# Kernel optimization log

Hardware: AMD Instinct MI355X
Metric: run time of the kernel (lower is better)

Reference implementation:

```python
import jax, jax.numpy as jnp
import numpy as np

N_NODES = 50000
N_EDGES = 400000
D = 128


def _rgg_layer(x, src, tgt, Wk, Wq, Wv, Ws, b, n_nodes):
    # Node-level projections (dense GEMMs, as in PyG which applies Linear before message passing)
    k = x @ Wk  # lin_key, gathered at targets
    q = x @ Wq  # lin_query, gathered at sources
    v = x @ Wv  # lin_value, gathered at sources
    # Per-edge gather + sigmoid gate + elementwise message
    eta = jax.nn.sigmoid(k[tgt] + q[src])  # [E, D]
    msg = eta * v[src]                      # [E, D]
    # Scatter-add aggregation to target nodes
    agg = jax.ops.segment_sum(msg, tgt, num_segments=n_nodes)
    # Root/skip connection + bias
    return agg + x @ Ws + b


def setup_inputs() -> dict:
    key = jax.random.key(0)
    ks = jax.random.split(key, 12)
    s = 1.0 / np.sqrt(D)
    x = jax.random.normal(ks[0], (N_NODES, D), dtype=jnp.float32)
    edge_index = jax.random.randint(ks[1], (2, N_EDGES), 0, N_NODES, dtype=jnp.int64)
    W = lambda k: (jax.random.normal(k, (D, D), dtype=jnp.float32) * s)
    return {
        "x": x,
        "edge_index": edge_index,
        "Wk1": W(ks[2]), "Wq1": W(ks[3]), "Wv1": W(ks[4]), "Ws1": W(ks[5]),
        "b1": jnp.zeros((D,), dtype=jnp.float32),
        "Wk2": W(ks[6]), "Wq2": W(ks[7]), "Wv2": W(ks[8]), "Ws2": W(ks[9]),
        "b2": jnp.zeros((D,), dtype=jnp.float32),
    }


def reference(x, edge_index, Wk1, Wq1, Wv1, Ws1, b1, Wk2, Wq2, Wv2, Ws2, b2):
    src, tgt = edge_index[0], edge_index[1]
    n = x.shape[0]
    h = _rgg_layer(x, src, tgt, Wk1, Wq1, Wv1, Ws1, b1, n)
    h = jax.nn.relu(h)
    # F.dropout treated as identity (deterministic/inference reference)
    out = _rgg_layer(h, src, tgt, Wk2, Wq2, Wv2, Ws2, b2, n)
    return out
```

## Files before the change

### kernel.cpp

```cpp
#include <hip/hip_runtime.h>

#define N_NODES 50000
#define D 128
#define N_EDGES 400000
#define NCHUNKS ((N_NODES + 255) / 256)
#define NBLK64 ((N_NODES + 63) / 64)
#define W_FRAG_SHORTS 16384

#define MW_BLOCKS  64
#define HIST_BLOCKS ((N_EDGES + 255) / 256)
#define PREP_BLOCKS (MW_BLOCKS + HIST_BLOCKS)

typedef short s8v  __attribute__((ext_vector_type(8)));
typedef float f4v  __attribute__((ext_vector_type(4)));

__device__ __forceinline__ unsigned int f2bf(float f) {
    unsigned int u = __float_as_uint(f);
    u += 0x7FFFu + ((u >> 16) & 1u);
    return u >> 16;
}
__device__ __forceinline__ unsigned int packbf(float a, float b) {
    return (f2bf(b) << 16) | f2bf(a);
}
__device__ __forceinline__ float bflo(unsigned int u) { return __uint_as_float(u << 16); }
__device__ __forceinline__ float bfhi(unsigned int u) { return __uint_as_float(u & 0xFFFF0000u); }
__device__ __forceinline__ float sigm(float x) {
    return __builtin_amdgcn_rcpf(1.f + __expf(-x));
}

__global__ __launch_bounds__(256)
void prep_all(const float* __restrict__ W0, const float* __restrict__ W1,
              const float* __restrict__ W2, const float* __restrict__ W3,
              const float* __restrict__ W4, const float* __restrict__ W5,
              const float* __restrict__ W6, const float* __restrict__ W7,
              short* __restrict__ Wt,
              const int* __restrict__ tgt, int* __restrict__ counts)
{
    const int b = blockIdx.x;
    if (b < MW_BLOCKS) {
        const int wsel = b >> 3;
        const float* W = (wsel == 0) ? W0 : (wsel == 1) ? W1 : (wsel == 2) ? W2 :
                         (wsel == 3) ? W3 : (wsel == 4) ? W4 : (wsel == 5) ? W5 :
                         (wsel == 6) ? W6 : W7;
        const int slot = (b & 7) * 256 + threadIdx.x;
        const int frag = slot >> 6;
        const int lane = slot & 63;
        const int n    = (frag >> 2) * 16 + (lane & 15);
        const int kc   = frag & 3;
        const int quad = lane >> 4;
        const int k0   = kc * 32 + quad * 8;
        s8v v;
#pragma unroll
        for (int j = 0; j < 8; ++j)
            v[j] = (short)f2bf(W[(size_t)(k0 + j) * D + n]);
        *(s8v*)(Wt + (size_t)wsel * W_FRAG_SHORTS + (size_t)slot * 8) = v;
    } else {
        const int e = (b - MW_BLOCKS) * 256 + threadIdx.x;
        if (e < N_EDGES) atomicAdd(&counts[tgt[e]], 1);
    }
}

__global__ __launch_bounds__(256)
void csr_scan(const int* __restrict__ counts, int* __restrict__ off,
              int* __restrict__ cursor, int* __restrict__ done_ctr,
              int* __restrict__ chunk_sum)
{
    __shared__ int s[256];
    const int b = blockIdx.x, t = threadIdx.x;
    const int i = b * 256 + t;
    const int v = (i < N_NODES) ? counts[i] : 0;
    s[t] = v;
    __syncthreads();
    for (int d = 1; d < 256; d <<= 1) {
        int tt = (t >= d) ? s[t - d] : 0;
        __syncthreads();
        s[t] += tt;
        __syncthreads();
    }
    const int incl = s[t];

    if (t == 255) {
        __hip_atomic_store(&chunk_sum[b], incl, __ATOMIC_RELAXED, __HIP_MEMORY_SCOPE_AGENT);
        __hip_atomic_fetch_add(done_ctr, 1, __ATOMIC_RELEASE, __HIP_MEMORY_SCOPE_AGENT);
    }
    if (t == 0) {
        while (__hip_atomic_load(done_ctr, __ATOMIC_ACQUIRE, __HIP_MEMORY_SCOPE_AGENT) < NCHUNKS)
            __builtin_amdgcn_s_sleep(8);
    }
    __syncthreads();

    const int pv = (t < b) ? __hip_atomic_load(&chunk_sum[t], __ATOMIC_RELAXED,
                                               __HIP_MEMORY_SCOPE_AGENT) : 0;
    __syncthreads();
    s[t] = pv;
    __syncthreads();
    for (int d = 128; d > 0; d >>= 1) {
        if (t < d) s[t] += s[t + d];
        __syncthreads();
    }
    const int base = s[0];

    if (i < N_NODES) {
        const int excl = base + incl - v;
        off[i]    = excl;
        cursor[i] = excl;
    }
    if (b == 0 && t == 0) off[N_NODES] = N_EDGES;
}

__device__ __forceinline__
void stage_b(const short* __restrict__ Wf, short* Bs, int tid)
{
#pragma unroll
    for (int j = 0; j < 8; ++j) {
        const int chunk = tid + 256 * j;
        __builtin_amdgcn_global_load_lds(
            (const __attribute__((address_space(1))) unsigned int*)(Wf + chunk * 8),
            (__attribute__((address_space(3))) unsigned int*)(&Bs[(chunk & ~63) * 8]),
            16, 0, 0);
    }
}

__device__ __forceinline__
void mfma_phase(const short* As, const short* Bs, int lane, int wr, int wc,
                f4v acc[2][4])
{
#pragma unroll
    for (int mt = 0; mt < 2; ++mt)
#pragma unroll
        for (int nt = 0; nt < 4; ++nt)
            acc[mt][nt] = (f4v){0.f, 0.f, 0.f, 0.f};
#pragma unroll
    for (int kc = 0; kc < 4; ++kc) {
        const int sl = (lane ^ (kc << 1)) * 8;
        s8v a0 = *(const s8v*)&As[((2 * wr + 0) * 4 + kc) * 512 + sl];
        s8v a1 = *(const s8v*)&As[((2 * wr + 1) * 4 + kc) * 512 + sl];
#pragma unroll
        for (int nt = 0; nt < 4; ++nt) {
            s8v b = *(const s8v*)&Bs[((4 * wc + nt) * 4 + kc) * 512 + lane * 8];
            acc[0][nt] = __builtin_amdgcn_mfma_f32_16x16x32_bf16(a0, b, acc[0][nt], 0, 0, 0);
            acc[1][nt] = __builtin_amdgcn_mfma_f32_16x16x32_bf16(a1, b, acc[1][nt], 0, 0, 0);
        }
    }
}

__device__ __forceinline__
void c_to_lds(float* Cs, int lane, int wr, int wc, const f4v acc[2][4])
{
#pragma unroll
    for (int mt = 0; mt < 2; ++mt) {
        const int r0 = wr * 32 + mt * 16 + (lane >> 4) * 4;
#pragma unroll
        for (int nt = 0; nt < 4; ++nt) {
            const int col = wc * 64 + nt * 16 + (lane & 15);
            const int g = col >> 2, jj = col & 3;
#pragma unroll
            for (int i = 0; i < 4; ++i) {
                const int row = r0 + i;
                const int gs  = g ^ (((row >> 2) & 3) << 2);
                Cs[row * 128 + gs * 4 + jj] = acc[mt][nt][i];
            }
        }
    }
}

template<bool X_FP32, bool AGG_BF16>
__device__ __forceinline__
void gemm_tile(int m0, const float* __restrict__ Xf, const short* __restrict__ Xb,
               const short* __restrict__ WtL, const float* __restrict__ bias,
               short* __restrict__ Kb, unsigned int* __restrict__ QV,
               float* __restrict__ AggF, unsigned int* __restrict__ AggB,
               short* As, short* Bs, float* biasS)
{
    const int tid  = threadIdx.x;
    const int lane = tid & 63;
    const int w    = tid >> 6;
    const int wr   = w & 1;
    const int wc   = w >> 1;

    if (tid < 128) biasS[tid] = bias[tid];

#pragma unroll
    for (int i = 0; i < 4; ++i) {
        const int m   = (tid >> 4) + 16 * i;
        const int oct = tid & 15;
        const int row = m0 + m;
        s8v v = (s8v){0, 0, 0, 0, 0, 0, 0, 0};
        if (row < N_NODES) {
            if (X_FP32) {
                const float* p = Xf + (size_t)row * D + oct * 8;
                float4 a0 = *(const float4*)p;
                float4 a1 = *(const float4*)(p + 4);
                v[0] = (short)f2bf(a0.x); v[1] = (short)f2bf(a0.y);
                v[2] = (short)f2bf(a0.z); v[3] = (short)f2bf(a0.w);
                v[4] = (short)f2bf(a1.x); v[5] = (short)f2bf(a1.y);
                v[6] = (short)f2bf(a1.z); v[7] = (short)f2bf(a1.w);
            } else {
                v = *(const s8v*)(Xb + (size_t)row * D + oct * 8);
            }
        }
        const int kc = oct >> 2, quad = oct & 3;
        const int frag = (m >> 4) * 4 + kc;
        const int slot = ((m & 15) + 16 * quad) ^ (kc << 1);
        *(s8v*)&As[frag * 512 + slot * 8] = v;
    }

    float* Cs = (float*)Bs;
    f4v acc[2][4];

    __syncthreads();
    stage_b(WtL + 0 * W_FRAG_SHORTS, Bs, tid);
    __syncthreads();
    mfma_phase(As, Bs, lane, wr, wc, acc);
    __syncthreads();
    c_to_lds(Cs, lane, wr, wc, acc);
    __syncthreads();
#pragma unroll
    for (int j = 0; j < 8; ++j) {
        const int c   = tid + 256 * j;
        const int row = c >> 5, gg = c & 31;
        const int gs  = gg ^ (((row >> 2) & 3) << 2);
        const f4v vv  = *(const f4v*)&Cs[row * 128 + gs * 4];
        const int grow = m0 + row;
        if (grow < N_NODES) {
            uint2* kp = (uint2*)((unsigned int*)Kb + (size_t)grow * 64 + gg * 2);
            *kp = make_uint2(packbf(vv[0], vv[1]), packbf(vv[2], vv[3]));
        }
    }

    f4v accV[2][4];
    __syncthreads();
    stage_b(WtL + 1 * W_FRAG_SHORTS, Bs, tid);
    __syncthreads();
    mfma_phase(As, Bs, lane, wr, wc, acc);
    __syncthreads();
    stage_b(WtL + 2 * W_FRAG_SHORTS, Bs, tid);
    __syncthreads();
    mfma_phase(As, Bs, lane, wr, wc, accV);
    __syncthreads();
    c_to_lds(Cs, lane, wr, wc, acc);
    __syncthreads();
    unsigned int qp0[8], qp1[8];
#pragma unroll
    for (int j = 0; j < 8; ++j) {
        const int c   = tid + 256 * j;
        const int row = c >> 5, gg = c & 31;
        const int gs  = gg ^ (((row >> 2) & 3) << 2);
        const f4v vv  = *(const f4v*)&Cs[row * 128 + gs * 4];
        qp0[j] = packbf(vv[0], vv[1]);
        qp1[j] = packbf(vv[2], vv[3]);
    }
    __syncthreads();
    c_to_lds(Cs, lane, wr, wc, accV);
    __syncthreads();
#pragma unroll
    for (int j = 0; j < 8; ++j) {
        const int c   = tid + 256 * j;
        const int row = c >> 5, gg = c & 31;
        const int gs  = gg ^ (((row >> 2) & 3) << 2);
        const f4v vv  = *(const f4v*)&Cs[row * 128 + gs * 4];
        const int grow = m0 + row;
        if (grow < N_NODES) {
            uint4* qvp = (uint4*)(QV + (size_t)grow * 128 + gg * 4);
            *qvp = make_uint4(qp0[j], packbf(vv[0], vv[1]),
                              qp1[j], packbf(vv[2], vv[3]));
        }
    }

    __syncthreads();
    stage_b(WtL + 3 * W_FRAG_SHORTS, Bs, tid);
    __syncthreads();
    mfma_phase(As, Bs, lane, wr, wc, acc);
    __syncthreads();
    c_to_lds(Cs, lane, wr, wc, acc);
    __syncthreads();
#pragma unroll
    for (int j = 0; j < 8; ++j) {
        const int c   = tid + 256 * j;
        const int row = c >> 5, gg = c & 31;
        const int gs  = gg ^ (((row >> 2) & 3) << 2);
        const f4v vv  = *(const f4v*)&Cs[row * 128 + gs * 4];
        const int grow = m0 + row;
        if (grow >= N_NODES) continue;
        const float4 bv = *(const float4*)&biasS[gg * 4];
        const float o0 = vv[0] + bv.x, o1 = vv[1] + bv.y;
        const float o2 = vv[2] + bv.z, o3 = vv[3] + bv.w;
        if (AGG_BF16) {
            uint2* ap = (uint2*)(AggB + (size_t)grow * 64 + gg * 2);
            *ap = make_uint2(packbf(o0, o1), packbf(o2, o3));
        } else {
            *(float4*)&AggF[(size_t)grow * D + gg * 4] = make_float4(o0, o1, o2, o3);
        }
    }
}

__global__ __launch_bounds__(256)
void gemm1_scatter(const float* __restrict__ X, const short* __restrict__ WtL,
                   const float* __restrict__ bias,
                   short* __restrict__ Kb, unsigned int* __restrict__ QV,
                   unsigned int* __restrict__ AggB,
                   const int* __restrict__ src, const int* __restrict__ tgt,
                   int* __restrict__ cursor, int* __restrict__ es)
{
    __shared__ __align__(16) short As[8192];
    __shared__ __align__(16) short Bs[16384];
    __shared__ __align__(16) float biasS[128];

    if (blockIdx.x < NBLK64) {
        gemm_tile<true, true>(blockIdx.x * 64, X, nullptr, WtL, bias,
                              Kb, QV, nullptr, AggB, As, Bs, biasS);
    } else {
        const int e = (blockIdx.x - NBLK64) * 256 + threadIdx.x;
        if (e < N_EDGES) {
            int pos = atomicAdd(&cursor[tgt[e]], 1);
            es[pos] = src[e];
        }
    }
}

__global__ __launch_bounds__(256)
void gemm2(const short* __restrict__ Hb, const short* __restrict__ WtL,
           const float* __restrict__ bias,
           short* __restrict__ Kb, unsigned int* __restrict__ QV,
           float* __restrict__ AggF)
{
    __shared__ __align__(16) short As[8192];
    __shared__ __align__(16) short Bs[16384];
    __shared__ __align__(16) float biasS[128];
    gemm_tile<false, false>(blockIdx.x * 64, nullptr, Hb, WtL, bias,
                            Kb, QV, AggF, nullptr, As, Bs, biasS);
}

template<bool FIRST>
__global__ __launch_bounds__(256)
void node_agg(const int* __restrict__ off, const int* __restrict__ es,
              const short* __restrict__ K, const unsigned int* __restrict__ QV,
              const void* __restrict__ Skip, float* __restrict__ OutF,
              unsigned int* __restrict__ Hb)
{
    const int lane = threadIdx.x & 63;
    const int t    = __builtin_amdgcn_readfirstlane(blockIdx.x * 4 + (threadIdx.x >> 6));

    const unsigned int ku = ((const unsigned int*)K)[(size_t)t * 64 + lane];
    const float kx = bflo(ku), ky = bfhi(ku);

    float skx, sky;
    if (FIRST) {
        const unsigned int su = ((const unsigned int*)Skip)[(size_t)t * 64 + lane];
        skx = bflo(su); sky = bfhi(su);
    } else {
        const float2 s2 = ((const float2*)Skip)[(size_t)t * 64 + lane];
        skx = s2.x; sky = s2.y;
    }

    float ax = 0.f, ay = 0.f, bx = 0.f, by = 0.f;
    const int e0 = __builtin_amdgcn_readfirstlane(off[t]);
    const int e1 = __builtin_amdgcn_readfirstlane(off[t + 1]);

    int e = e0;
    for (; e + 8 <= e1; e += 8) {
        const int sv = es[e + (lane & 7)];
        uint2 g[8];
#pragma unroll
        for (int u = 0; u < 8; ++u) {
            const int s = __builtin_amdgcn_readlane(sv, u);
            g[u] = ((const uint2*)(QV + (size_t)s * 128))[lane];
        }
#pragma unroll
        for (int u = 0; u < 8; ++u) {
            if (u & 1) {
                bx += bflo(g[u].y) * sigm(kx + bflo(g[u].x));
                by += bfhi(g[u].y) * sigm(ky + bfhi(g[u].x));
            } else {
                ax += bflo(g[u].y) * sigm(kx + bflo(g[u].x));
                ay += bfhi(g[u].y) * sigm(ky + bfhi(g[u].x));
            }
        }
    }
    if (e + 4 <= e1) {
        const int sv = es[e + (lane & 3)];
        uint2 g[4];
#pragma unroll
        for (int u = 0; u < 4; ++u) {
            const int s = __builtin_amdgcn_readlane(sv, u);
            g[u] = ((const uint2*)(QV + (size_t)s * 128))[lane];
        }
#pragma unroll
        for (int u = 0; u < 4; ++u) {
            if (u & 1) {
                bx += bflo(g[u].y) * sigm(kx + bflo(g[u].x));
                by += bfhi(g[u].y) * sigm(ky + bfhi(g[u].x));
            } else {
                ax += bflo(g[u].y) * sigm(kx + bflo(g[u].x));
                ay += bfhi(g[u].y) * sigm(ky + bfhi(g[u].x));
            }
        }
        e += 4;
    }
    for (; e < e1; ++e) {
        const int s0 = __builtin_amdgcn_readfirstlane(es[e]);
        const uint2 g0 = ((const uint2*)(QV + (size_t)s0 * 128))[lane];
        ax += bflo(g0.y) * sigm(kx + bflo(g0.x));
        ay += bfhi(g0.y) * sigm(ky + bfhi(g0.x));
    }

    const float rx = skx + ax + bx;
    const float ry = sky + ay + by;

    if (FIRST) {
        Hb[(size_t)t * 64 + lane] = packbf(fmaxf(rx, 0.f), fmaxf(ry, 0.f));
    } else {
        ((float2*)OutF)[(size_t)t * 64 + lane] = make_float2(rx, ry);
    }
}

extern "C" void kernel_launch(void* const* d_in, const int* in_sizes, int n_in,
                              void* d_out, int out_size, void* d_ws, size_t ws_size,
                              hipStream_t stream)
{
    const float* x   = (const float*)d_in[0];
    const int*   ei  = (const int*)d_in[1];
    const float* Wk1 = (const float*)d_in[2];
    const float* Wq1 = (const float*)d_in[3];
    const float* Wv1 = (const float*)d_in[4];
    const float* Ws1 = (const float*)d_in[5];
    const float* b1  = (const float*)d_in[6];
    const float* Wk2 = (const float*)d_in[7];
    const float* Wq2 = (const float*)d_in[8];
    const float* Wv2 = (const float*)d_in[9];
    const float* Ws2 = (const float*)d_in[10];
    const float* b2  = (const float*)d_in[11];

    const int* src = ei;
    const int* tgt = ei + N_EDGES;

    const size_t nd = (size_t)N_NODES * D;
    short* kb   = (short*)d_ws;
    short* qv   = kb + nd;
    short* hb   = qv + 2 * nd;
    short* ag1  = hb + nd;
    short* wt   = ag1 + nd;
    int* counts    = (int*)(wt + 8 * W_FRAG_SHORTS);
    int* done_ctr  = counts + N_NODES;
    int* off       = counts + N_NODES + 2;
    int* cursor    = off + N_NODES + 1;
    int* es        = cursor + N_NODES;
    int* chunk_sum = es + N_EDGES;
    float* out = (float*)d_out;

    hipMemsetAsync(counts, 0, (N_NODES + 2) * sizeof(int), stream);
    prep_all<<<PREP_BLOCKS, 256, 0, stream>>>(Wk1, Wq1, Wv1, Ws1, Wk2, Wq2, Wv2, Ws2,
                                              wt, tgt, counts);
    csr_scan<<<NCHUNKS, 256, 0, stream>>>(counts, off, cursor, done_ctr, chunk_sum);

    gemm1_scatter<<<NBLK64 + HIST_BLOCKS, 256, 0, stream>>>(
        x, wt, b1, kb, (unsigned int*)qv, (unsigned int*)ag1, src, tgt, cursor, es);
    node_agg<true><<<N_NODES / 4, 256, 0, stream>>>(off, es, kb, (const unsigned int*)qv,
                                                    ag1, nullptr, (unsigned int*)hb);

    gemm2<<<NBLK64, 256, 0, stream>>>(hb, wt + 4 * W_FRAG_SHORTS, b2,
                                      kb, (unsigned int*)qv, out);
    node_agg<false><<<N_NODES / 4, 256, 0, stream>>>(off, es, kb, (const unsigned int*)qv,
                                                     out, out, nullptr);
}
```

Measured before the change: 255.8 us.

## Shrink GEMM tile to 32 rows and load weight fragments directly into registers

The node-projection GEMM tiles drop from 64 to 32 rows. Each wave now covers all 32 rows and a 32-column slice, and reads its weight fragments straight from global memory into registers, so the LDS staging of the weight matrix and several barriers go away. LDS use per block drops and launch bounds request 4 blocks per CU, aiming for higher occupancy and less synchronisation. The cost is that weights are re-read from global or L2 for every tile, which doubles the number of tiles and so the total weight traffic.

Result: no change. 256.5 us (+0.3%).

```diff
diff --git a/kernel.cpp b/kernel.cpp
--- a/kernel.cpp
+++ b/kernel.cpp
@@ -4,7 +4,7 @@
 #define D 128
 #define N_EDGES 400000
 #define NCHUNKS ((N_NODES + 255) / 256)
-#define NBLK64 ((N_NODES + 63) / 64)
+#define NBLK32 ((N_NODES + 31) / 32)
 #define W_FRAG_SHORTS 16384
 
 #define MW_BLOCKS  64
@@ -109,56 +109,48 @@
 }
 
 __device__ __forceinline__
-void stage_b(const short* __restrict__ Wf, short* Bs, int tid)
-{
-#pragma unroll
-    for (int j = 0; j < 8; ++j) {
-        const int chunk = tid + 256 * j;
-        __builtin_amdgcn_global_load_lds(
-            (const __attribute__((address_space(1))) unsigned int*)(Wf + chunk * 8),
-            (__attribute__((address_space(3))) unsigned int*)(&Bs[(chunk & ~63) * 8]),
-            16, 0, 0);
-    }
-}
-
-__device__ __forceinline__
-void mfma_phase(const short* As, const short* Bs, int lane, int wr, int wc,
-                f4v acc[2][4])
-{
+void mfma_phase32(const short* As, const short* __restrict__ Wf,
+                  int lane, int w, f4v acc[2][2])
+{
+    s8v bv[2][4];
+#pragma unroll
+    for (int nt2 = 0; nt2 < 2; ++nt2)
+#pragma unroll
+        for (int kc = 0; kc < 4; ++kc)
+            bv[nt2][kc] = *(const s8v*)(Wf + (((2 * w + nt2) * 4 + kc) * 64 + lane) * 8);
 #pragma unroll
     for (int mt = 0; mt < 2; ++mt)
 #pragma unroll
-        for (int nt = 0; nt < 4; ++nt)
-            acc[mt][nt] = (f4v){0.f, 0.f, 0.f, 0.f};
+        for (int nt2 = 0; nt2 < 2; ++nt2)
+            acc[mt][nt2] = (f4v){0.f, 0.f, 0.f, 0.f};
 #pragma unroll
     for (int kc = 0; kc < 4; ++kc) {
         const int sl = (lane ^ (kc << 1)) * 8;
-        s8v a0 = *(const s8v*)&As[((2 * wr + 0) * 4 + kc) * 512 + sl];
-        s8v a1 = *(const s8v*)&As[((2 * wr + 1) * 4 + kc) * 512 + sl];
-#pragma unroll
-        for (int nt = 0; nt < 4; ++nt) {
-            s8v b = *(const s8v*)&Bs[((4 * wc + nt) * 4 + kc) * 512 + lane * 8];
-            acc[0][nt] = __builtin_amdgcn_mfma_f32_16x16x32_bf16(a0, b, acc[0][nt], 0, 0, 0);
-            acc[1][nt] = __builtin_amdgcn_mfma_f32_16x16x32_bf16(a1, b, acc[1][nt], 0, 0, 0);
+        s8v a0 = *(const s8v*)&As[(0 * 4 + kc) * 512 + sl];
+        s8v a1 = *(const s8v*)&As[(1 * 4 + kc) * 512 + sl];
+#pragma unroll
+        for (int nt2 = 0; nt2 < 2; ++nt2) {
+            acc[0][nt2] = __builtin_amdgcn_mfma_f32_16x16x32_bf16(a0, bv[nt2][kc], acc[0][nt2], 0, 0, 0);
+            acc[1][nt2] = __builtin_amdgcn_mfma_f32_16x16x32_bf16(a1, bv[nt2][kc], acc[1][nt2], 0, 0, 0);
         }
     }
 }
 
 __device__ __forceinline__
-void c_to_lds(float* Cs, int lane, int wr, int wc, const f4v acc[2][4])
+void c_to_lds32(float* Cs, int lane, int w, const f4v acc[2][2])
 {
 #pragma unroll
     for (int mt = 0; mt < 2; ++mt) {
-        const int r0 = wr * 32 + mt * 16 + (lane >> 4) * 4;
-#pragma unroll
-        for (int nt = 0; nt < 4; ++nt) {
-            const int col = wc * 64 + nt * 16 + (lane & 15);
+        const int r0 = mt * 16 + (lane >> 4) * 4;
+#pragma unroll
+        for (int nt2 = 0; nt2 < 2; ++nt2) {
+            const int col = w * 32 + nt2 * 16 + (lane & 15);
             const int g = col >> 2, jj = col & 3;
 #pragma unroll
             for (int i = 0; i < 4; ++i) {
                 const int row = r0 + i;
                 const int gs  = g ^ (((row >> 2) & 3) << 2);
-                Cs[row * 128 + gs * 4 + jj] = acc[mt][nt][i];
+                Cs[row * 128 + gs * 4 + jj] = acc[mt][nt2][i];
             }
         }
     }
@@ -170,18 +162,16 @@
                const short* __restrict__ WtL, const float* __restrict__ bias,
                short* __restrict__ Kb, unsigned int* __restrict__ QV,
                float* __restrict__ AggF, unsigned int* __restrict__ AggB,
-               short* As, short* Bs, float* biasS)
+               short* As, float* Cs, float* biasS)
 {
     const int tid  = threadIdx.x;
     const int lane = tid & 63;
     const int w    = tid >> 6;
-    const int wr   = w & 1;
-    const int wc   = w >> 1;
 
     if (tid < 128) biasS[tid] = bias[tid];
 
 #pragma unroll
-    for (int i = 0; i < 4; ++i) {
+    for (int i = 0; i < 2; ++i) {
         const int m   = (tid >> 4) + 16 * i;
         const int oct = tid & 15;
         const int row = m0 + m;
@@ -205,18 +195,14 @@
         *(s8v*)&As[frag * 512 + slot * 8] = v;
     }
 
-    float* Cs = (float*)Bs;
-    f4v acc[2][4];
-
-    __syncthreads();
-    stage_b(WtL + 0 * W_FRAG_SHORTS, Bs, tid);
-    __syncthreads();
-    mfma_phase(As, Bs, lane, wr, wc, acc);
-    __syncthreads();
-    c_to_lds(Cs, lane, wr, wc, acc);
-    __syncthreads();
-#pragma unroll
-    for (int j = 0; j < 8; ++j) {
+    f4v acc[2][2], accV[2][2];
+    __syncthreads();
+
+    mfma_phase32(As, WtL + 0 * W_FRAG_SHORTS, lane, w, acc);
+    c_to_lds32(Cs, lane, w, acc);
+    __syncthreads();
+#pragma unroll
+    for (int j = 0; j < 4; ++j) {
         const int c   = tid + 256 * j;
         const int row = c >> 5, gg = c & 31;
         const int gs  = gg ^ (((row >> 2) & 3) << 2);
@@ -227,22 +213,15 @@
             *kp = make_uint2(packbf(vv[0], vv[1]), packbf(vv[2], vv[3]));
         }
     }
-
-    f4v accV[2][4];
-    __syncthreads();
-    stage_b(WtL + 1 * W_FRAG_SHORTS, Bs, tid);
-    __syncthreads();
-    mfma_phase(As, Bs, lane, wr, wc, acc);
-    __syncthreads();
-    stage_b(WtL + 2 * W_FRAG_SHORTS, Bs, tid);
-    __syncthreads();
-    mfma_phase(As, Bs, lane, wr, wc, accV);
-    __syncthreads();
-    c_to_lds(Cs, lane, wr, wc, acc);
-    __syncthreads();
-    unsigned int qp0[8], qp1[8];
-#pragma unroll
-    for (int j = 0; j < 8; ++j) {
+    __syncthreads();
+
+    mfma_phase32(As, WtL + 1 * W_FRAG_SHORTS, lane, w, acc);
+    mfma_phase32(As, WtL + 2 * W_FRAG_SHORTS, lane, w, accV);
+    c_to_lds32(Cs, lane, w, acc);
+    __syncthreads();
+    unsigned int qp0[4], qp1[4];
+#pragma unroll
+    for (int j = 0; j < 4; ++j) {
         const int c   = tid + 256 * j;
         const int row = c >> 5, gg = c & 31;
         const int gs  = gg ^ (((row >> 2) & 3) << 2);
@@ -251,10 +230,10 @@
         qp1[j] = packbf(vv[2], vv[3]);
     }
     __syncthreads();
-    c_to_lds(Cs, lane, wr, wc, accV);
-    __syncthreads();
-#pragma unroll
-    for (int j = 0; j < 8; ++j) {
+    c_to_lds32(Cs, lane, w, accV);
+    __syncthreads();
+#pragma unroll
+    for (int j = 0; j < 4; ++j) {
         const int c   = tid + 256 * j;
         const int row = c >> 5, gg = c & 31;
         const int gs  = gg ^ (((row >> 2) & 3) << 2);
@@ -266,16 +245,13 @@
                               qp1[j], packbf(vv[2], vv[3]));
         }
     }
-
-    __syncthreads();
-    stage_b(WtL + 3 * W_FRAG_SHORTS, Bs, tid);
-    __syncthreads();
-    mfma_phase(As, Bs, lane, wr, wc, acc);
-    __syncthreads();
-    c_to_lds(Cs, lane, wr, wc, acc);
-    __syncthreads();
-#pragma unroll
-    for (int j = 0; j < 8; ++j) {
+    __syncthreads();
+
+    mfma_phase32(As, WtL + 3 * W_FRAG_SHORTS, lane, w, acc);
+    c_to_lds32(Cs, lane, w, acc);
+    __syncthreads();
+#pragma unroll
+    for (int j = 0; j < 4; ++j) {
         const int c   = tid + 256 * j;
         const int row = c >> 5, gg = c & 31;
         const int gs  = gg ^ (((row >> 2) & 3) << 2);
@@ -294,7 +270,7 @@
     }
 }
 
-__global__ __launch_bounds__(256)
+__global__ __launch_bounds__(256, 4)
 void gemm1_scatter(const float* __restrict__ X, const short* __restrict__ WtL,
                    const float* __restrict__ bias,
                    short* __restrict__ Kb, unsigned int* __restrict__ QV,
@@ -302,15 +278,15 @@
                    const int* __restrict__ src, const int* __restrict__ tgt,
                    int* __restrict__ cursor, int* __restrict__ es)
 {
-    __shared__ __align__(16) short As[8192];
-    __shared__ __align__(16) short Bs[16384];
+    __shared__ __align__(16) short As[4096];
+    __shared__ __align__(16) float Cs[4096];
     __shared__ __align__(16) float biasS[128];
 
-    if (blockIdx.x < NBLK64) {
-        gemm_tile<true, true>(blockIdx.x * 64, X, nullptr, WtL, bias,
-                              Kb, QV, nullptr, AggB, As, Bs, biasS);
+    if (blockIdx.x < NBLK32) {
+        gemm_tile<true, true>(blockIdx.x * 32, X, nullptr, WtL, bias,
+                              Kb, QV, nullptr, AggB, As, Cs, biasS);
     } else {
-        const int e = (blockIdx.x - NBLK64) * 256 + threadIdx.x;
+        const int e = (blockIdx.x - NBLK32) * 256 + threadIdx.x;
         if (e < N_EDGES) {
             int pos = atomicAdd(&cursor[tgt[e]], 1);
             es[pos] = src[e];
@@ -318,17 +294,17 @@
     }
 }
 
-__global__ __launch_bounds__(256)
+__global__ __launch_bounds__(256, 4)
 void gemm2(const short* __restrict__ Hb, const short* __restrict__ WtL,
            const float* __restrict__ bias,
            short* __restrict__ Kb, unsigned int* __restrict__ QV,
            float* __restrict__ AggF)
 {
-    __shared__ __align__(16) short As[8192];
-    __shared__ __align__(16) short Bs[16384];
+    __shared__ __align__(16) short As[4096];
+    __shared__ __align__(16) float Cs[4096];
     __shared__ __align__(16) float biasS[128];
-    gemm_tile<false, false>(blockIdx.x * 64, nullptr, Hb, WtL, bias,
-                            Kb, QV, AggF, nullptr, As, Bs, biasS);
+    gemm_tile<false, false>(blockIdx.x * 32, nullptr, Hb, WtL, bias,
+                            Kb, QV, AggF, nullptr, As, Cs, biasS);
 }
 
 template<bool FIRST>
@@ -453,12 +429,12 @@
                                               wt, tgt, counts);
     csr_scan<<<NCHUNKS, 256, 0, stream>>>(counts, off, cursor, done_ctr, chunk_sum);
 
-    gemm1_scatter<<<NBLK64 + HIST_BLOCKS, 256, 0, stream>>>(
+    gemm1_scatter<<<NBLK32 + HIST_BLOCKS, 256, 0, stream>>>(
         x, wt, b1, kb, (unsigned int*)qv, (unsigned int*)ag1, src, tgt, cursor, es);
     node_agg<true><<<N_NODES / 4, 256, 0, stream>>>(off, es, kb, (const unsigned int*)qv,
                                                     ag1, nullptr, (unsigned int*)hb);
 
-    gemm2<<<NBLK64, 256, 0, stream>>>(hb, wt + 4 * W_FRAG_SHORTS, b2,
+    gemm2<<<NBLK32, 256, 0, stream>>>(hb, wt + 4 * W_FRAG_SHORTS, b2,
                                       kb, (unsigned int*)qv, out);
     node_agg<false><<<N_NODES / 4, 256, 0, stream>>>(off, es, kb, (const unsigned int*)qv,
                                                      out, out, nullptr);
```

## Use 32-row GEMM tiles with direct-global B fragments for layer two; reorder scatter blocks

Applied to the files above, without the earlier changes.

Layer two's GEMM moves from 64-row to 32-row tiles. It reads weight fragments straight from global memory into registers instead of staging them in LDS, which shrinks shared memory and raises occupancy through launch_bounds(256,4). The scatter blocks in gemm1_scatter are now placed ahead of the GEMM blocks so the atomics start earlier. The cost is more blocks and repeated weight reads from L2 or global memory per block.

Result: slower. 262.2 us (+2.5%).

```diff
diff --git a/kernel.cpp b/kernel.cpp
--- a/kernel.cpp
+++ b/kernel.cpp
@@ -5,6 +5,7 @@
 #define N_EDGES 400000
 #define NCHUNKS ((N_NODES + 255) / 256)
 #define NBLK64 ((N_NODES + 63) / 64)
+#define NBLK32 ((N_NODES + 31) / 31 == 0 ? 0 : (N_NODES + 31) / 32)
 #define W_FRAG_SHORTS 16384
 
 #define MW_BLOCKS  64
@@ -164,13 +165,12 @@
     }
 }
 
-template<bool X_FP32, bool AGG_BF16>
-__device__ __forceinline__
-void gemm_tile(int m0, const float* __restrict__ Xf, const short* __restrict__ Xb,
-               const short* __restrict__ WtL, const float* __restrict__ bias,
-               short* __restrict__ Kb, unsigned int* __restrict__ QV,
-               float* __restrict__ AggF, unsigned int* __restrict__ AggB,
-               short* As, short* Bs, float* biasS)
+__device__ __forceinline__
+void gemm_tile64(int m0, const float* __restrict__ Xf,
+                 const short* __restrict__ WtL, const float* __restrict__ bias,
+                 short* __restrict__ Kb, unsigned int* __restrict__ QV,
+                 unsigned int* __restrict__ AggB,
+                 short* As, short* Bs, float* biasS)
 {
     const int tid  = threadIdx.x;
     const int lane = tid & 63;
@@ -187,17 +187,13 @@
         const int row = m0 + m;
         s8v v = (s8v){0, 0, 0, 0, 0, 0, 0, 0};
         if (row < N_NODES) {
-            if (X_FP32) {
-                const float* p = Xf + (size_t)row * D + oct * 8;
-                float4 a0 = *(const float4*)p;
-                float4 a1 = *(const float4*)(p + 4);
-                v[0] = (short)f2bf(a0.x); v[1] = (short)f2bf(a0.y);
-                v[2] = (short)f2bf(a0.z); v[3] = (short)f2bf(a0.w);
-                v[4] = (short)f2bf(a1.x); v[5] = (short)f2bf(a1.y);
-                v[6] = (short)f2bf(a1.z); v[7] = (short)f2bf(a1.w);
-            } else {
-                v = *(const s8v*)(Xb + (size_t)row * D + oct * 8);
-            }
+            const float* p = Xf + (size_t)row * D + oct * 8;
+            float4 a0 = *(const float4*)p;
+            float4 a1 = *(const float4*)(p + 4);
+            v[0] = (short)f2bf(a0.x); v[1] = (short)f2bf(a0.y);
+            v[2] = (short)f2bf(a0.z); v[3] = (short)f2bf(a0.w);
+            v[4] = (short)f2bf(a1.x); v[5] = (short)f2bf(a1.y);
+            v[6] = (short)f2bf(a1.z); v[7] = (short)f2bf(a1.w);
         }
         const int kc = oct >> 2, quad = oct & 3;
         const int frag = (m >> 4) * 4 + kc;
@@ -283,14 +279,153 @@
         const int grow = m0 + row;
         if (grow >= N_NODES) continue;
         const float4 bv = *(const float4*)&biasS[gg * 4];
-        const float o0 = vv[0] + bv.x, o1 = vv[1] + bv.y;
-        const float o2 = vv[2] + bv.z, o3 = vv[3] + bv.w;
-        if (AGG_BF16) {
-            uint2* ap = (uint2*)(AggB + (size_t)grow * 64 + gg * 2);
-            *ap = make_uint2(packbf(o0, o1), packbf(o2, o3));
-        } else {
-            *(float4*)&AggF[(size_t)grow * D + gg * 4] = make_float4(o0, o1, o2, o3);
-        }
+        uint2* ap = (uint2*)(AggB + (size_t)grow * 64 + gg * 2);
+        *ap = make_uint2(packbf(vv[0] + bv.x, vv[1] + bv.y),
+                         packbf(vv[2] + bv.z, vv[3] + bv.w));
+    }
+}
+
+__device__ __forceinline__
+void mfma_phase32(const short* As, const short* __restrict__ Wf,
+                  int lane, int w, f4v acc[2][2])
+{
+    s8v bv[2][4];
+#pragma unroll
+    for (int nt2 = 0; nt2 < 2; ++nt2)
+#pragma unroll
+        for (int kc = 0; kc < 4; ++kc)
+            bv[nt2][kc] = *(const s8v*)(Wf + (((2 * w + nt2) * 4 + kc) * 64 + lane) * 8);
+#pragma unroll
+    for (int mt = 0; mt < 2; ++mt)
+#pragma unroll
+        for (int nt2 = 0; nt2 < 2; ++nt2)
+            acc[mt][nt2] = (f4v){0.f, 0.f, 0.f, 0.f};
+#pragma unroll
+    for (int kc = 0; kc < 4; ++kc) {
+        const int sl = (lane ^ (kc << 1)) * 8;
+        s8v a0 = *(const s8v*)&As[(0 * 4 + kc) * 512 + sl];
+        s8v a1 = *(const s8v*)&As[(1 * 4 + kc) * 512 + sl];
+#pragma unroll
+        for (int nt2 = 0; nt2 < 2; ++nt2) {
+            acc[0][nt2] = __builtin_amdgcn_mfma_f32_16x16x32_bf16(a0, bv[nt2][kc], acc[0][nt2], 0, 0, 0);
+            acc[1][nt2] = __builtin_amdgcn_mfma_f32_16x16x32_bf16(a1, bv[nt2][kc], acc[1][nt2], 0, 0, 0);
+        }
+    }
+}
+
+__device__ __forceinline__
+void c_to_lds32(float* Cs, int lane, int w, const f4v acc[2][2])
+{
+#pragma unroll
+    for (int mt = 0; mt < 2; ++mt) {
+        const int r0 = mt * 16 + (lane >> 4) * 4;
+#pragma unroll
+        for (int nt2 = 0; nt2 < 2; ++nt2) {
+            const int col = w * 32 + nt2 * 16 + (lane & 15);
+            const int g = col >> 2, jj = col & 3;
+#pragma unroll
+            for (int i = 0; i < 4; ++i) {
+                const int row = r0 + i;
+                const int gs  = g ^ (((row >> 2) & 3) << 2);
+                Cs[row * 128 + gs * 4 + jj] = acc[mt][nt2][i];
+            }
+        }
+    }
+}
+
+__device__ __forceinline__
+void gemm_tile32(int m0, const short* __restrict__ Xb,
+                 const short* __restrict__ WtL, const float* __restrict__ bias,
+                 short* __restrict__ Kb, unsigned int* __restrict__ QV,
+                 float* __restrict__ AggF,
+                 short* As, float* Cs, float* biasS)
+{
+    const int tid  = threadIdx.x;
+    const int lane = tid & 63;
+    const int w    = tid >> 6;
+
+    if (tid < 128) biasS[tid] = bias[tid];
+
+#pragma unroll
+    for (int i = 0; i < 2; ++i) {
+        const int m   = (tid >> 4) + 16 * i;
+        const int oct = tid & 15;
+        const int row = m0 + m;
+        s8v v = (s8v){0, 0, 0, 0, 0, 0, 0, 0};
+        if (row < N_NODES)
+            v = *(const s8v*)(Xb + (size_t)row * D + oct * 8);
+        const int kc = oct >> 2, quad = oct & 3;
+        const int frag = (m >> 4) * 4 + kc;
+        const int slot = ((m & 15) + 16 * quad) ^ (kc << 1);
+        *(s8v*)&As[frag * 512 + slot * 8] = v;
+    }
+
+    f4v acc[2][2], accV[2][2];
+    __syncthreads();
+
+    mfma_phase32(As, WtL + 0 * W_FRAG_SHORTS, lane, w, acc);
+    c_to_lds32(Cs, lane, w, acc);
+    __syncthreads();
+#pragma unroll
+    for (int j = 0; j < 4; ++j) {
+        const int c   = tid + 256 * j;
+        const int row = c >> 5, gg = c & 31;
+        const int gs  = gg ^ (((row >> 2) & 3) << 2);
+        const f4v vv  = *(const f4v*)&Cs[row * 128 + gs * 4];
+        const int grow = m0 + row;
+        if (grow < N_NODES) {
+            uint2* kp = (uint2*)((unsigned int*)Kb + (size_t)grow * 64 + gg * 2);
+            *kp = make_uint2(packbf(vv[0], vv[1]), packbf(vv[2], vv[3]));
+        }
+    }
+    __syncthreads();
+
+    mfma_phase32(As, WtL + 1 * W_FRAG_SHORTS, lane, w, acc);
+    mfma_phase32(As, WtL + 2 * W_FRAG_SHORTS, lane, w, accV);
+    c_to_lds32(Cs, lane, w, acc);
+    __syncthreads();
+    unsigned int qp0[4], qp1[4];
+#pragma unroll
+    for (int j = 0; j < 4; ++j) {
+        const int c   = tid + 256 * j;
+        const int row = c >> 5, gg = c & 31;
+        const int gs  = gg ^ (((row >> 2) & 3) << 2);
+        const f4v vv  = *(const f4v*)&Cs[row * 128 + gs * 4];
+        qp0[j] = packbf(vv[0], vv[1]);
+        qp1[j] = packbf(vv[2], vv[3]);
+    }
+    __syncthreads();
+    c_to_lds32(Cs, lane, w, accV);
+    __syncthreads();
+#pragma unroll
+    for (int j = 0; j < 4; ++j) {
+        const int c   = tid + 256 * j;
+        const int row = c >> 5, gg = c & 31;
+        const int gs  = gg ^ (((row >> 2) & 3) << 2);
+        const f4v vv  = *(const f4v*)&Cs[row * 128 + gs * 4];
+        const int grow = m0 + row;
+        if (grow < N_NODES) {
+            uint4* qvp = (uint4*)(QV + (size_t)grow * 128 + gg * 4);
+            *qvp = make_uint4(qp0[j], packbf(vv[0], vv[1]),
+                              qp1[j], packbf(vv[2], vv[3]));
+        }
+    }
+    __syncthreads();
+
+    mfma_phase32(As, WtL + 3 * W_FRAG_SHORTS, lane, w, acc);
+    c_to_lds32(Cs, lane, w, acc);
+    __syncthreads();
+#pragma unroll
+    for (int j = 0; j < 4; ++j) {
+        const int c   = tid + 256 * j;
+        const int row = c >> 5, gg = c & 31;
+        const int gs  = gg ^ (((row >> 2) & 3) << 2);
+        const f4v vv  = *(const f4v*)&Cs[row * 128 + gs * 4];
+        const int grow = m0 + row;
+        if (grow >= N_NODES) continue;
+        const float4 bv = *(const float4*)&biasS[gg * 4];
+        *(float4*)&AggF[(size_t)grow * D + gg * 4] =
+            make_float4(vv[0] + bv.x, vv[1] + bv.y, vv[2] + bv.z, vv[3] + bv.w);
     }
 }
 
@@ -306,11 +441,11 @@
     __shared__ __align__(16) short Bs[16384];
     __shared__ __align__(16) float biasS[128];
 
-    if (blockIdx.x < NBLK64) {
-        gemm_tile<true, true>(blockIdx.x * 64, X, nullptr, WtL, bias,
-                              Kb, QV, nullptr, AggB, As, Bs, biasS);
+    if (blockIdx.x >= HIST_BLOCKS) {
+        gemm_tile64((blockIdx.x - HIST_BLOCKS) * 64, X, WtL, bias,
+                    Kb, QV, AggB, As, Bs, biasS);
     } else {
-        const int e = (blockIdx.x - NBLK64) * 256 + threadIdx.x;
+        const int e = blockIdx.x * 256 + threadIdx.x;
         if (e < N_EDGES) {
             int pos = atomicAdd(&cursor[tgt[e]], 1);
             es[pos] = src[e];
@@ -318,17 +453,16 @@
     }
 }
 
-__global__ __launch_bounds__(256)
+__global__ __launch_bounds__(256, 4)
 void gemm2(const short* __restrict__ Hb, const short* __restrict__ WtL,
            const float* __restrict__ bias,
            short* __restrict__ Kb, unsigned int* __restrict__ QV,
            float* __restrict__ AggF)
 {
-    __shared__ __align__(16) short As[8192];
-    __shared__ __align__(16) short Bs[16384];
+    __shared__ __align__(16) short As[4096];
+    __shared__ __align__(16) float Cs[4096];
     __shared__ __align__(16) float biasS[128];
-    gemm_tile<false, false>(blockIdx.x * 64, nullptr, Hb, WtL, bias,
-                            Kb, QV, AggF, nullptr, As, Bs, biasS);
+    gemm_tile32(blockIdx.x * 32, Hb, WtL, bias, Kb, QV, AggF, As, Cs, biasS);
 }
 
 template<bool FIRST>
@@ -453,12 +587,12 @@
                                               wt, tgt, counts);
     csr_scan<<<NCHUNKS, 256, 0, stream>>>(counts, off, cursor, done_ctr, chunk_sum);
 
-    gemm1_scatter<<<NBLK64 + HIST_BLOCKS, 256, 0, stream>>>(
+    gemm1_scatter<<<HIST_BLOCKS + NBLK64, 256, 0, stream>>>(
         x, wt, b1, kb, (unsigned int*)qv, (unsigned int*)ag1, src, tgt, cursor, es);
     node_agg<true><<<N_NODES / 4, 256, 0, stream>>>(off, es, kb, (const unsigned int*)qv,
                                                     ag1, nullptr, (unsigned int*)hb);
 
-    gemm2<<<NBLK64, 256, 0, stream>>>(hb, wt + 4 * W_FRAG_SHORTS, b2,
+    gemm2<<<NBLK32, 256, 0, stream>>>(hb, wt + 4 * W_FRAG_SHORTS, b2,
                                       kb, (unsigned int*)qv, out);
     node_agg<false><<<N_NODES / 4, 256, 0, stream>>>(off, es, kb, (const unsigned int*)qv,
                                                      out, out, nullptr);
```
